# Optimization experiments

Hardware: AMD Instinct MI355X
Metric: run time of the kernel (lower is better)

Reference implementation:

```python
import jax, jax.numpy as jnp
import numpy as np
import math

H_HEADS = 16
D_PER = 64
D_MODEL = 1024
B, L = 8, 1024


def _dual_attention(q1, k1, q2, k2, v):
    # all [B,h,L,d]; scores = avg of two scaled QK^T
    scale = 1.0 / math.sqrt(q1.shape[-1])
    s1 = jnp.einsum('bhqd,bhkd->bhqk', q1, k1) * scale
    s2 = jnp.einsum('bhqd,bhkd->bhqk', q2, k2) * scale
    p = jax.nn.softmax((s1 + s2) * 0.5, axis=-1)
    return jnp.einsum('bhqk,bhkd->bhqd', p, v)


def _proj(X, W, b):
    # [B,L,D] -> [B,h,L,d]
    Bb, Ll, _ = X.shape
    y = X @ W + b
    return y.reshape(Bb, Ll, H_HEADS, D_PER).transpose(0, 2, 1, 3)


def _mha(Q1, K1, Q2, K2, V, Wq, bq, Wk, bk, Wv, bv, Wo, bo):
    q1 = _proj(Q1, Wq, bq)
    k1 = _proj(K1, Wk, bk)
    q2 = _proj(Q2, Wq, bq)  # same linear as q1 (linears[0])
    k2 = _proj(K2, Wk, bk)  # same linear as k1 (linears[1])
    v = _proj(V, Wv, bv)
    o = _dual_attention(q1, k1, q2, k2, v)  # [B,h,L,d]
    Bb = o.shape[0]
    o = o.transpose(0, 2, 1, 3).reshape(Bb, -1, H_HEADS * D_PER)
    return o @ Wo + bo  # [B,L,D]


def setup_inputs() -> dict:
    key = jax.random.key(0)
    ks = jax.random.split(key, 5)
    sc = 1.0 / math.sqrt(D_MODEL)
    return {
        'x': jax.random.normal(ks[0], (B, L, 3, D_MODEL), jnp.float32),
        'Wq': jax.random.normal(ks[1], (D_MODEL, H_HEADS * D_PER), jnp.float32) * sc,
        'bq': jnp.zeros((H_HEADS * D_PER,), jnp.float32),
        'Wk': jax.random.normal(ks[2], (D_MODEL, H_HEADS * D_PER), jnp.float32) * sc,
        'bk': jnp.zeros((H_HEADS * D_PER,), jnp.float32),
        'Wv': jax.random.normal(ks[3], (D_MODEL, H_HEADS * D_PER), jnp.float32) * sc,
        'bv': jnp.zeros((H_HEADS * D_PER,), jnp.float32),
        'Wo': jax.random.normal(ks[4], (H_HEADS * D_PER, D_MODEL), jnp.float32) * sc,
        'bo': jnp.zeros((D_MODEL,), jnp.float32),
    }


def reference(x, Wq, bq, Wk, bk, Wv, bv, Wo, bo):
    Hx = x[:, :, 0, :]
    Tx = x[:, :, 1, :]
    Rx = x[:, :, 2, :]
    p = (Wq, bq, Wk, bk, Wv, bv, Wo, bo)
    H_new = _mha(Tx, Tx, Rx, Rx, Hx, *p)
    T_new = _mha(Hx, Hx, Rx, Rx, Tx, *p)
    R_new = _mha(Hx, Hx, Tx, Tx, Rx, *p)
    return jnp.stack([H_new, T_new, R_new], axis=2)  # [B,L,3,D]
```

## Files before the change

kernel.cpp:

```cpp
#include <hip/hip_runtime.h>
#include <hip/hip_bf16.h>
#include <stdint.h>

#define NTOK 8192
#define DM   1024

typedef __bf16 bf16x8 __attribute__((ext_vector_type(8)));
typedef float  f32x4  __attribute__((ext_vector_type(4)));

__device__ __forceinline__ unsigned short f2bf(float f) {
  union { float f; unsigned u; } v; v.f = f;
  unsigned r = v.u + 0x7FFFu + ((v.u >> 16) & 1u);
  return (unsigned short)(r >> 16);
}

__device__ __forceinline__ void gld16(const void* g, const void* l) {
  __builtin_amdgcn_global_load_lds(
      (const __attribute__((address_space(1))) uint32_t*)g,
      (__attribute__((address_space(3))) uint32_t*)l, 16, 0, 0);
}

__global__ void convert_x(const float* __restrict__ x, unsigned short* __restrict__ Xbf) {
  int idx = (blockIdx.x * 256 + threadIdx.x) * 4;
  int s   = idx >> 23;
  int rem = idx & ((1 << 23) - 1);
  int tok = rem >> 10;
  int d   = rem & 1023;
  const float4 v = *(const float4*)&x[((size_t)tok * 3 + s) * 1024 + d];
  ushort4 o;
  o.x = f2bf(v.x); o.y = f2bf(v.y); o.z = f2bf(v.z); o.w = f2bf(v.w);
  *(ushort4*)&Xbf[idx] = o;
}

__global__ void transpose_w(const float* __restrict__ W, unsigned short* __restrict__ Wt) {
  __shared__ float t[32][33];
  int tx = threadIdx.x, ty = threadIdx.y;
  int bx = blockIdx.x * 32, by = blockIdx.y * 32;
#pragma unroll
  for (int i = 0; i < 32; i += 8)
    t[ty + i][tx] = W[(size_t)(by + ty + i) * 1024 + bx + tx];
  __syncthreads();
#pragma unroll
  for (int i = 0; i < 32; i += 8)
    Wt[(size_t)(bx + ty + i) * 1024 + by + tx] = f2bf(t[tx][ty + i]);
}

__device__ __forceinline__ void gemm128_core(
    const unsigned short* __restrict__ A, const unsigned short* __restrict__ Bt,
    unsigned short* lA, unsigned short* lB, f32x4 acc[4][4])
{
  int tid  = threadIdx.x;
  int wave = tid >> 6, lane = tid & 63, quad = lane >> 4, l16 = lane & 15;
  int m0 = blockIdx.x * 128, n0 = blockIdx.y * 128;
  int r0 = tid >> 2;
  int kc = (((tid & 3) ^ ((tid >> 3) & 3)) * 8);
  const unsigned short* Ag = A  + (size_t)(m0 + r0) * 1024 + kc;
  const unsigned short* Bg = Bt + (size_t)(n0 + r0) * 1024 + kc;
  int wm = (wave >> 1) * 64, wn = (wave & 1) * 64;
  int fsw = (l16 >> 1) & 3;

  for (int k0 = 0; k0 < 1024; k0 += 32) {
    gld16(Ag + k0,             lA + wave * 512);
    gld16(Ag + k0 + 64 * 1024, lA + 2048 + wave * 512);
    gld16(Bg + k0,             lB + wave * 512);
    gld16(Bg + k0 + 64 * 1024, lB + 2048 + wave * 512);
    __syncthreads();
    bf16x8 af[4], bfr[4];
    int fo = ((quad ^ fsw) * 8);
#pragma unroll
    for (int i = 0; i < 4; i++) {
      af[i]  = *(const bf16x8*)&lA[(wm + i * 16 + l16) * 32 + fo];
      bfr[i] = *(const bf16x8*)&lB[(wn + i * 16 + l16) * 32 + fo];
    }
#pragma unroll
    for (int mi = 0; mi < 4; mi++)
#pragma unroll
      for (int ni = 0; ni < 4; ni++)
        acc[mi][ni] = __builtin_amdgcn_mfma_f32_16x16x32_bf16(af[mi], bfr[ni], acc[mi][ni], 0, 0, 0);
    __syncthreads();
  }
}

__global__ __launch_bounds__(256, 2) void gemm_proj(
    const unsigned short* __restrict__ Xbf, const unsigned short* __restrict__ Wt,
    unsigned short* __restrict__ P,
    const float* __restrict__ bq, const float* __restrict__ bk, const float* __restrict__ bv)
{
  __shared__ alignas(16) unsigned short lA[128 * 32];
  __shared__ alignas(16) unsigned short lB[128 * 32];
  int z = blockIdx.z, s = z / 3, w = z - s * 3;
  const float* bias = (w == 0) ? bq : (w == 1) ? bk : bv;
  f32x4 acc[4][4];
#pragma unroll
  for (int i = 0; i < 4; i++)
#pragma unroll
    for (int j = 0; j < 4; j++) acc[i][j] = (f32x4){0.f, 0.f, 0.f, 0.f};
  gemm128_core(Xbf + (size_t)s * NTOK * 1024, Wt + (size_t)w * 1024 * 1024, lA, lB, acc);

  int tid = threadIdx.x, wave = tid >> 6, lane = tid & 63, quad = lane >> 4, l16 = lane & 15;
  int m0 = blockIdx.x * 128 + (wave >> 1) * 64;
  int n0 = blockIdx.y * 128 + (wave & 1) * 64;
  unsigned short* C = P + (size_t)z * NTOK * 1024;
  if (w == 2) {
#pragma unroll
    for (int mi = 0; mi < 4; mi++) {
      int row0 = m0 + mi * 16 + quad * 4;
      int b = row0 >> 10, l0 = row0 & 1023;
#pragma unroll
      for (int ni = 0; ni < 4; ni++) {
        int col = n0 + ni * 16 + l16;
        float bcol = bias[col];
        int hh = col >> 6, d = col & 63;
        ushort4 o4;
        o4.x = f2bf(acc[mi][ni][0] + bcol);
        o4.y = f2bf(acc[mi][ni][1] + bcol);
        o4.z = f2bf(acc[mi][ni][2] + bcol);
        o4.w = f2bf(acc[mi][ni][3] + bcol);
        *(ushort4*)&C[(size_t)(b * 16 + hh) * 65536 + (size_t)d * 1024 + l0] = o4;
      }
    }
  } else {
#pragma unroll
    for (int mi = 0; mi < 4; mi++)
#pragma unroll
      for (int ni = 0; ni < 4; ni++) {
        int col = n0 + ni * 16 + l16;
        float bcol = bias[col];
#pragma unroll
        for (int r = 0; r < 4; r++) {
          int row = m0 + mi * 16 + quad * 4 + r;
          C[(size_t)row * 1024 + col] = f2bf(acc[mi][ni][r] + bcol);
        }
      }
  }
}

__global__ __launch_bounds__(256, 4) void attn(
    const unsigned short* __restrict__ P, unsigned short* __restrict__ Oa)
{
  __shared__ alignas(16) unsigned short lK1[64 * 64];
  __shared__ alignas(16) unsigned short lK2[64 * 64];
  __shared__ alignas(16) unsigned short lV [64 * 64];
  __shared__ alignas(16) unsigned short pls[4][32 * 40];
  int o  = blockIdx.z;
  int As = (o == 0) ? 1 : 0;
  int Bs = (o == 2) ? 1 : 2;
  int b = blockIdx.x >> 4, h = blockIdx.x & 15;
  int tid = threadIdx.x, wave = tid >> 6, lane = tid & 63, quad = lane >> 4, l16 = lane & 15;
  int q0 = blockIdx.y * 128 + wave * 32;
  size_t bh_off = (size_t)b * 1024 * 1024 + h * 64;
  const unsigned short* Q1 = P + (size_t)(As * 3 + 0) * NTOK * 1024 + bh_off;
  const unsigned short* K1 = P + (size_t)(As * 3 + 1) * NTOK * 1024 + bh_off;
  const unsigned short* Q2 = P + (size_t)(Bs * 3 + 0) * NTOK * 1024 + bh_off;
  const unsigned short* K2 = P + (size_t)(Bs * 3 + 1) * NTOK * 1024 + bh_off;
  const unsigned short* V  = P + (size_t)(o * 3 + 2) * NTOK * 1024
                               + (size_t)(b * 16 + h) * 65536;
  unsigned short* myp = pls[wave];

  bf16x8 q1f[2][2], q2f[2][2];
#pragma unroll
  for (int qt = 0; qt < 2; qt++)
#pragma unroll
    for (int c = 0; c < 2; c++) {
      q1f[qt][c] = *(const bf16x8*)&Q1[(size_t)(q0 + qt * 16 + l16) * 1024 + c * 32 + quad * 8];
      q2f[qt][c] = *(const bf16x8*)&Q2[(size_t)(q0 + qt * 16 + l16) * 1024 + c * 32 + quad * 8];
    }
  bf16x8 ones;
#pragma unroll
  for (int j = 0; j < 8; j++) ones[j] = (__bf16)1.0f;

  int r8 = lane >> 3;
  int cs = ((lane & 7) ^ r8) * 8;
  int srow = wave * 16 + r8;
  const unsigned short* K1s = K1 + (size_t)srow * 1024 + cs;
  const unsigned short* K2s = K2 + (size_t)srow * 1024 + cs;
  const unsigned short* Vs  = V  + (size_t)srow * 1024 + cs;
  int fsw = (l16 & 7);

  f32x4 oacc[2][4];
#pragma unroll
  for (int qt = 0; qt < 2; qt++)
#pragma unroll
    for (int dt = 0; dt < 4; dt++) oacc[qt][dt] = (f32x4){0.f, 0.f, 0.f, 0.f};
  f32x4 lsum[2];
  lsum[0] = (f32x4){0.f, 0.f, 0.f, 0.f};
  lsum[1] = (f32x4){0.f, 0.f, 0.f, 0.f};

  const float SC = 0.09016844136867f;

  for (int k0 = 0; k0 < 1024; k0 += 64) {
#pragma unroll
    for (int half = 0; half < 2; half++) {
      size_t krow = (size_t)(k0 + half * 8) * 1024;
      gld16(K1s + krow,                 lK1 + (wave * 16 + half * 8) * 64);
      gld16(K2s + krow,                 lK2 + (wave * 16 + half * 8) * 64);
      gld16(Vs + k0 + half * 8 * 1024,  lV  + (wave * 16 + half * 8) * 64);
    }
    __syncthreads();

#pragma unroll
    for (int kc = 0; kc < 2; kc++) {
      f32x4 sacc[2][2];
      sacc[0][0] = (f32x4){0.f, 0.f, 0.f, 0.f};
      sacc[0][1] = (f32x4){0.f, 0.f, 0.f, 0.f};
      sacc[1][0] = (f32x4){0.f, 0.f, 0.f, 0.f};
      sacc[1][1] = (f32x4){0.f, 0.f, 0.f, 0.f};
      __builtin_amdgcn_s_setprio(1);
#pragma unroll
      for (int kt = 0; kt < 2; kt++) {
        int krow = (kc * 32 + kt * 16 + l16) * 64;
        bf16x8 k1a = *(const bf16x8*)&lK1[krow + ((quad ^ fsw) * 8)];
        bf16x8 k1b = *(const bf16x8*)&lK1[krow + (((quad + 4) ^ fsw) * 8)];
        bf16x8 k2a = *(const bf16x8*)&lK2[krow + ((quad ^ fsw) * 8)];
        bf16x8 k2b = *(const bf16x8*)&lK2[krow + (((quad + 4) ^ fsw) * 8)];
#pragma unroll
        for (int qt = 0; qt < 2; qt++) {
          sacc[qt][kt] = __builtin_amdgcn_mfma_f32_16x16x32_bf16(q1f[qt][0], k1a, sacc[qt][kt], 0, 0, 0);
          sacc[qt][kt] = __builtin_amdgcn_mfma_f32_16x16x32_bf16(q1f[qt][1], k1b, sacc[qt][kt], 0, 0, 0);
          sacc[qt][kt] = __builtin_amdgcn_mfma_f32_16x16x32_bf16(q2f[qt][0], k2a, sacc[qt][kt], 0, 0, 0);
          sacc[qt][kt] = __builtin_amdgcn_mfma_f32_16x16x32_bf16(q2f[qt][1], k2b, sacc[qt][kt], 0, 0, 0);
        }
      }
      __builtin_amdgcn_s_setprio(0);
#pragma unroll
      for (int qt = 0; qt < 2; qt++)
#pragma unroll
        for (int kt = 0; kt < 2; kt++)
#pragma unroll
          for (int r2 = 0; r2 < 2; r2++) {
            union { float f; unsigned u; } e0, e1;
            e0.f = __builtin_amdgcn_exp2f(sacc[qt][kt][r2 * 2]     * SC);
            e1.f = __builtin_amdgcn_exp2f(sacc[qt][kt][r2 * 2 + 1] * SC);
            unsigned pk = __builtin_amdgcn_perm(e1.u + 0x8000u, e0.u + 0x8000u, 0x07060302u);
            int row = qt * 16 + quad * 4 + r2 * 2;
            myp[row * 40 + kt * 16 + l16]       = (unsigned short)pk;
            myp[(row + 1) * 40 + kt * 16 + l16] = (unsigned short)(pk >> 16);
          }
      bf16x8 pa0 = *(const bf16x8*)&myp[l16 * 40 + quad * 8];
      bf16x8 pa1 = *(const bf16x8*)&myp[(16 + l16) * 40 + quad * 8];
      __builtin_amdgcn_s_setprio(1);
      lsum[0] = __builtin_amdgcn_mfma_f32_16x16x32_bf16(pa0, ones, lsum[0], 0, 0, 0);
      lsum[1] = __builtin_amdgcn_mfma_f32_16x16x32_bf16(pa1, ones, lsum[1], 0, 0, 0);
#pragma unroll
      for (int dt = 0; dt < 4; dt++) {
        bf16x8 vf = *(const bf16x8*)&lV[(dt * 16 + l16) * 64 + (((kc * 4 + quad) ^ fsw) * 8)];
        oacc[0][dt] = __builtin_amdgcn_mfma_f32_16x16x32_bf16(pa0, vf, oacc[0][dt], 0, 0, 0);
        oacc[1][dt] = __builtin_amdgcn_mfma_f32_16x16x32_bf16(pa1, vf, oacc[1][dt], 0, 0, 0);
      }
      __builtin_amdgcn_s_setprio(0);
    }
    __syncthreads();
  }

  unsigned short* Od = Oa + (size_t)o * NTOK * 1024 + bh_off;
#pragma unroll
  for (int qt = 0; qt < 2; qt++) {
    f32x4 inv;
#pragma unroll
    for (int r = 0; r < 4; r++) inv[r] = 1.0f / lsum[qt][r];
#pragma unroll
    for (int dt = 0; dt < 4; dt++)
#pragma unroll
      for (int r = 0; r < 4; r++) {
        float val = oacc[qt][dt][r] * inv[r];
        Od[(size_t)(q0 + qt * 16 + quad * 4 + r) * 1024 + dt * 16 + l16] = f2bf(val);
      }
  }
}

__global__ __launch_bounds__(256, 2) void gemm_out(
    const unsigned short* __restrict__ Oattn, const unsigned short* __restrict__ WtO,
    float* __restrict__ out, const float* __restrict__ bo)
{
  __shared__ alignas(16) unsigned short lA[128 * 32];
  __shared__ alignas(16) unsigned short lB[128 * 32];
  int s = blockIdx.z;
  f32x4 acc[4][4];
#pragma unroll
  for (int i = 0; i < 4; i++)
#pragma unroll
    for (int j = 0; j < 4; j++) acc[i][j] = (f32x4){0.f, 0.f, 0.f, 0.f};
  gemm128_core(Oattn + (size_t)s * NTOK * 1024, WtO, lA, lB, acc);

  int tid = threadIdx.x, wave = tid >> 6, lane = tid & 63, quad = lane >> 4, l16 = lane & 15;
  int m0 = blockIdx.x * 128 + (wave >> 1) * 64;
  int n0 = blockIdx.y * 128 + (wave & 1) * 64;
#pragma unroll
  for (int mi = 0; mi < 4; mi++)
#pragma unroll
    for (int ni = 0; ni < 4; ni++) {
      int col = n0 + ni * 16 + l16;
      float bcol = bo[col];
#pragma unroll
      for (int r = 0; r < 4; r++) {
        int row = m0 + mi * 16 + quad * 4 + r;
        out[(size_t)row * 3072 + s * 1024 + col] = acc[mi][ni][r] + bcol;
      }
    }
}

extern "C" void kernel_launch(void* const* d_in, const int* in_sizes, int n_in,
                              void* d_out, int out_size, void* d_ws, size_t ws_size,
                              hipStream_t stream) {
  (void)in_sizes; (void)n_in; (void)out_size; (void)ws_size;
  const float* x  = (const float*)d_in[0];
  const float* Wq = (const float*)d_in[1];
  const float* bq = (const float*)d_in[2];
  const float* Wk = (const float*)d_in[3];
  const float* bk = (const float*)d_in[4];
  const float* Wv = (const float*)d_in[5];
  const float* bv = (const float*)d_in[6];
  const float* Wo = (const float*)d_in[7];
  const float* bo = (const float*)d_in[8];
  float* out = (float*)d_out;

  char* ws = (char*)d_ws;
  unsigned short* Xbf = (unsigned short*)(ws + 0);
  unsigned short* Wt  = (unsigned short*)(ws + 50331648);
  unsigned short* P   = (unsigned short*)(ws + 58720256);
  unsigned short* Oa  = (unsigned short*)(ws + 209715200);

  convert_x<<<24576, 256, 0, stream>>>(x, Xbf);
  dim3 tb(32, 8), tg(32, 32);
  transpose_w<<<tg, tb, 0, stream>>>(Wq, Wt + 0 * 1048576);
  transpose_w<<<tg, tb, 0, stream>>>(Wk, Wt + 1 * 1048576);
  transpose_w<<<tg, tb, 0, stream>>>(Wv, Wt + 2 * 1048576);
  transpose_w<<<tg, tb, 0, stream>>>(Wo, Wt + 3 * 1048576);

  gemm_proj<<<dim3(64, 8, 9), 256, 0, stream>>>(Xbf, Wt, P, bq, bk, bv);
  attn<<<dim3(128, 8, 3), 256, 0, stream>>>(P, Oa);
  gemm_out<<<dim3(64, 8, 3), 256, 0, stream>>>(Oa, Wt + 3 * 1048576, out, bo);
}
```

Before: 614.2 us.

## Replace 128x128 GEMM core with pipelined 256x256 eight-wave tile core

Both projection and output GEMMs now use a 256x256 tile with 512 threads, K-step 64, double-buffered LDS staging via global_load_lds, and an interleaved schedule of LDS reads, async prefetches and MFMA quarters separated by barriers with raised wave priority. Blocks are also remapped with a swizzle to improve L2 reuse of A/B panels. The aim is to raise arithmetic intensity per LDS/global load and hide load latency behind MFMA work, at the cost of 128KB LDS per block, heavy register pressure, and fragile hand-tuned waitcnt/barrier ordering.

```diff
diff --git a/kernel.cpp b/kernel.cpp
--- a/kernel.cpp
+++ b/kernel.cpp
@@ -45,70 +45,130 @@
     Wt[(size_t)(bx + ty + i) * 1024 + by + tx] = f2bf(t[tx][ty + i]);
 }
 
-__device__ __forceinline__ void gemm128_core(
+#define STG_A(tt, d, hf) do { \
+  gld16(Ag + (size_t)((hf) * 128) * 1024 + (tt) * 64,      &lds[((d)*2+(hf))*8192 + wave*512]); \
+  gld16(Ag + (size_t)((hf) * 128 + 64) * 1024 + (tt) * 64, &lds[((d)*2+(hf))*8192 + wave*512 + 4096]); \
+} while (0)
+#define STG_B(tt, d, hf) do { \
+  gld16(Bg + (size_t)((hf) * 128) * 1024 + (tt) * 64,      &lds[32768 + ((d)*2+(hf))*8192 + wave*512]); \
+  gld16(Bg + (size_t)((hf) * 128 + 64) * 1024 + (tt) * 64, &lds[32768 + ((d)*2+(hf))*8192 + wave*512 + 4096]); \
+} while (0)
+#define RD_AG(g, d) do { \
+  const unsigned short* _p = &lds[((d)*2 + wm) * 8192]; \
+  _Pragma("unroll") for (int m2 = 0; m2 < 4; ++m2) \
+  _Pragma("unroll") for (int ks = 0; ks < 2; ++ks) \
+    af[(g)*4 + m2][ks] = *(const bf16x8*)&_p[((g)*4 + m2)*1024 + l16*64 + (((ks*4 + quad) ^ sw8) * 8)]; \
+} while (0)
+#define RD_BG(g, d) do { \
+  const unsigned short* _p = &lds[32768 + ((d)*2 + (wn >> 1)) * 8192 + (wn & 1) * 4096]; \
+  _Pragma("unroll") for (int n2 = 0; n2 < 2; ++n2) \
+  _Pragma("unroll") for (int ks = 0; ks < 2; ++ks) \
+    bfr[(g)*2 + n2][ks] = *(const bf16x8*)&_p[((g)*2 + n2)*1024 + l16*64 + (((ks*4 + quad) ^ sw8) * 8)]; \
+} while (0)
+#define MM_Q(qm, qn) do { \
+  __builtin_amdgcn_s_setprio(1); \
+  _Pragma("unroll") for (int m2 = 0; m2 < 4; ++m2) \
+  _Pragma("unroll") for (int n2 = 0; n2 < 2; ++n2) \
+  _Pragma("unroll") for (int ks = 0; ks < 2; ++ks) \
+    acc[(qm)*4 + m2][(qn)*2 + n2] = __builtin_amdgcn_mfma_f32_16x16x32_bf16( \
+      af[(qm)*4 + m2][ks], bfr[(qn)*2 + n2][ks], acc[(qm)*4 + m2][(qn)*2 + n2], 0, 0, 0); \
+  __builtin_amdgcn_s_setprio(0); \
+} while (0)
+#define PBAR() do { __builtin_amdgcn_s_barrier(); __builtin_amdgcn_sched_barrier(0); } while (0)
+#define WLGK0() do { asm volatile("s_waitcnt lgkmcnt(0)" ::: "memory"); __builtin_amdgcn_sched_barrier(0); } while (0)
+
+__device__ __forceinline__ void gemm256_core(
     const unsigned short* __restrict__ A, const unsigned short* __restrict__ Bt,
-    unsigned short* lA, unsigned short* lB, f32x4 acc[4][4])
+    unsigned short* lds, f32x4 acc[8][4], int m0, int n0)
 {
-  int tid  = threadIdx.x;
+  int tid = threadIdx.x;
   int wave = tid >> 6, lane = tid & 63, quad = lane >> 4, l16 = lane & 15;
-  int m0 = blockIdx.x * 128, n0 = blockIdx.y * 128;
-  int r0 = tid >> 2;
-  int kc = (((tid & 3) ^ ((tid >> 3) & 3)) * 8);
-  const unsigned short* Ag = A  + (size_t)(m0 + r0) * 1024 + kc;
-  const unsigned short* Bg = Bt + (size_t)(n0 + r0) * 1024 + kc;
-  int wm = (wave >> 1) * 64, wn = (wave & 1) * 64;
-  int fsw = (l16 >> 1) & 3;
-
-  for (int k0 = 0; k0 < 1024; k0 += 32) {
-    gld16(Ag + k0,             lA + wave * 512);
-    gld16(Ag + k0 + 64 * 1024, lA + 2048 + wave * 512);
-    gld16(Bg + k0,             lB + wave * 512);
-    gld16(Bg + k0 + 64 * 1024, lB + 2048 + wave * 512);
-    __syncthreads();
-    bf16x8 af[4], bfr[4];
-    int fo = ((quad ^ fsw) * 8);
-#pragma unroll
-    for (int i = 0; i < 4; i++) {
-      af[i]  = *(const bf16x8*)&lA[(wm + i * 16 + l16) * 32 + fo];
-      bfr[i] = *(const bf16x8*)&lB[(wn + i * 16 + l16) * 32 + fo];
-    }
-#pragma unroll
-    for (int mi = 0; mi < 4; mi++)
-#pragma unroll
-      for (int ni = 0; ni < 4; ni++)
-        acc[mi][ni] = __builtin_amdgcn_mfma_f32_16x16x32_bf16(af[mi], bfr[ni], acc[mi][ni], 0, 0, 0);
-    __syncthreads();
+  int wm = wave >> 2, wn = wave & 3;
+  int sw8 = l16 & 7;
+  int srow = wave * 8 + (lane >> 3);
+  int schk = ((lane & 7) ^ (lane >> 3)) * 8;
+  const unsigned short* Ag = A  + (size_t)(m0 + srow) * 1024 + schk;
+  const unsigned short* Bg = Bt + (size_t)(n0 + srow) * 1024 + schk;
+  bf16x8 af[8][2], bfr[4][2];
+
+  STG_A(0, 0, 0); STG_A(0, 0, 1); STG_B(0, 0, 0); STG_B(0, 0, 1);
+  STG_A(1, 1, 0); STG_A(1, 1, 1); STG_B(1, 1, 0);
+  asm volatile("s_waitcnt vmcnt(6)" ::: "memory");
+  PBAR();
+
+  for (int t = 0; t < 16; t += 2) {
+    RD_AG(0, 0); RD_BG(0, 0);
+    STG_B(t + 1, 1, 1);
+    __builtin_amdgcn_s_barrier(); WLGK0();
+    MM_Q(0, 0);
+    PBAR();
+    RD_AG(1, 0);
+    __builtin_amdgcn_s_barrier(); WLGK0();
+    MM_Q(1, 0);
+    PBAR();
+    RD_BG(1, 0);
+    if (t + 2 < 16) { STG_A(t + 2, 0, 0); STG_A(t + 2, 0, 1); }
+    __builtin_amdgcn_s_barrier(); WLGK0();
+    MM_Q(0, 1);
+    PBAR();
+    if (t + 2 < 16) STG_B(t + 2, 0, 0);
+    __builtin_amdgcn_s_barrier(); __builtin_amdgcn_sched_barrier(0);
+    MM_Q(1, 1);
+    if (t + 2 < 16) { asm volatile("s_waitcnt vmcnt(6)" ::: "memory"); }
+    else            { asm volatile("s_waitcnt vmcnt(0)" ::: "memory"); }
+    PBAR();
+    RD_AG(0, 1); RD_BG(0, 1);
+    if (t + 2 < 16) STG_B(t + 2, 0, 1);
+    __builtin_amdgcn_s_barrier(); WLGK0();
+    MM_Q(0, 0);
+    PBAR();
+    RD_AG(1, 1);
+    __builtin_amdgcn_s_barrier(); WLGK0();
+    MM_Q(1, 0);
+    PBAR();
+    RD_BG(1, 1);
+    if (t + 3 < 16) { STG_A(t + 3, 1, 0); STG_A(t + 3, 1, 1); }
+    __builtin_amdgcn_s_barrier(); WLGK0();
+    MM_Q(0, 1);
+    PBAR();
+    if (t + 3 < 16) STG_B(t + 3, 1, 0);
+    __builtin_amdgcn_s_barrier(); __builtin_amdgcn_sched_barrier(0);
+    MM_Q(1, 1);
+    if (t + 3 < 16) { asm volatile("s_waitcnt vmcnt(6)" ::: "memory"); }
+    PBAR();
   }
 }
 
-__global__ __launch_bounds__(256, 2) void gemm_proj(
+__global__ __launch_bounds__(512, 2) void gemm_proj(
     const unsigned short* __restrict__ Xbf, const unsigned short* __restrict__ Wt,
     unsigned short* __restrict__ P,
     const float* __restrict__ bq, const float* __restrict__ bk, const float* __restrict__ bv)
 {
-  __shared__ alignas(16) unsigned short lA[128 * 32];
-  __shared__ alignas(16) unsigned short lB[128 * 32];
+  __shared__ alignas(16) unsigned short lds[65536];
   int z = blockIdx.z, s = z / 3, w = z - s * 3;
   const float* bias = (w == 0) ? bq : (w == 1) ? bk : bv;
-  f32x4 acc[4][4];
-#pragma unroll
-  for (int i = 0; i < 4; i++)
+  int f = blockIdx.x;
+  int swz = (f & 7) * 16 + (f >> 3);
+  int m0 = (swz & 31) * 256, n0 = (swz >> 5) * 256;
+  f32x4 acc[8][4];
+#pragma unroll
+  for (int i = 0; i < 8; i++)
 #pragma unroll
     for (int j = 0; j < 4; j++) acc[i][j] = (f32x4){0.f, 0.f, 0.f, 0.f};
-  gemm128_core(Xbf + (size_t)s * NTOK * 1024, Wt + (size_t)w * 1024 * 1024, lA, lB, acc);
+  gemm256_core(Xbf + (size_t)s * NTOK * 1024, Wt + (size_t)w * 1048576, lds, acc, m0, n0);
 
   int tid = threadIdx.x, wave = tid >> 6, lane = tid & 63, quad = lane >> 4, l16 = lane & 15;
-  int m0 = blockIdx.x * 128 + (wave >> 1) * 64;
-  int n0 = blockIdx.y * 128 + (wave & 1) * 64;
+  int wm = wave >> 2, wn = wave & 3;
+  int rbase = m0 + wm * 128, cbase = n0 + wn * 64;
   unsigned short* C = P + (size_t)z * NTOK * 1024;
   if (w == 2) {
 #pragma unroll
-    for (int mi = 0; mi < 4; mi++) {
-      int row0 = m0 + mi * 16 + quad * 4;
+    for (int mi = 0; mi < 8; mi++) {
+      int row0 = rbase + mi * 16 + quad * 4;
       int b = row0 >> 10, l0 = row0 & 1023;
 #pragma unroll
       for (int ni = 0; ni < 4; ni++) {
-        int col = n0 + ni * 16 + l16;
+        int col = cbase + ni * 16 + l16;
         float bcol = bias[col];
         int hh = col >> 6, d = col & 63;
         ushort4 o4;
@@ -121,18 +181,51 @@
     }
   } else {
 #pragma unroll
-    for (int mi = 0; mi < 4; mi++)
+    for (int mi = 0; mi < 8; mi++)
 #pragma unroll
       for (int ni = 0; ni < 4; ni++) {
-        int col = n0 + ni * 16 + l16;
+        int col = cbase + ni * 16 + l16;
         float bcol = bias[col];
 #pragma unroll
         for (int r = 0; r < 4; r++) {
-          int row = m0 + mi * 16 + quad * 4 + r;
+          int row = rbase + mi * 16 + quad * 4 + r;
           C[(size_t)row * 1024 + col] = f2bf(acc[mi][ni][r] + bcol);
         }
       }
   }
+}
+
+__global__ __launch_bounds__(512, 2) void gemm_out(
+    const unsigned short* __restrict__ Oattn, const unsigned short* __restrict__ WtO,
+    float* __restrict__ out, const float* __restrict__ bo)
+{
+  __shared__ alignas(16) unsigned short lds[65536];
+  int s = blockIdx.z;
+  int f = blockIdx.x;
+  int swz = (f & 7) * 16 + (f >> 3);
+  int m0 = (swz & 31) * 256, n0 = (swz >> 5) * 256;
+  f32x4 acc[8][4];
+#pragma unroll
+  for (int i = 0; i < 8; i++)
+#pragma unroll
+    for (int j = 0; j < 4; j++) acc[i][j] = (f32x4){0.f, 0.f, 0.f, 0.f};
+  gemm256_core(Oattn + (size_t)s * NTOK * 1024, WtO, lds, acc, m0, n0);
+
+  int tid = threadIdx.x, wave = tid >> 6, lane = tid & 63, quad = lane >> 4, l16 = lane & 15;
+  int wm = wave >> 2, wn = wave & 3;
+  int rbase = m0 + wm * 128, cbase = n0 + wn * 64;
+#pragma unroll
+  for (int mi = 0; mi < 8; mi++)
+#pragma unroll
+    for (int ni = 0; ni < 4; ni++) {
+      int col = cbase + ni * 16 + l16;
+      float bcol = bo[col];
+#pragma unroll
+      for (int r = 0; r < 4; r++) {
+        int row = rbase + mi * 16 + quad * 4 + r;
+        out[(size_t)row * 3072 + s * 1024 + col] = acc[mi][ni][r] + bcol;
+      }
+    }
 }
 
 __global__ __launch_bounds__(256, 4) void attn(
@@ -268,37 +361,6 @@
   }
 }
 
-__global__ __launch_bounds__(256, 2) void gemm_out(
-    const unsigned short* __restrict__ Oattn, const unsigned short* __restrict__ WtO,
-    float* __restrict__ out, const float* __restrict__ bo)
-{
-  __shared__ alignas(16) unsigned short lA[128 * 32];
-  __shared__ alignas(16) unsigned short lB[128 * 32];
-  int s = blockIdx.z;
-  f32x4 acc[4][4];
-#pragma unroll
-  for (int i = 0; i < 4; i++)
-#pragma unroll
-    for (int j = 0; j < 4; j++) acc[i][j] = (f32x4){0.f, 0.f, 0.f, 0.f};
-  gemm128_core(Oattn + (size_t)s * NTOK * 1024, WtO, lA, lB, acc);
-
-  int tid = threadIdx.x, wave = tid >> 6, lane = tid & 63, quad = lane >> 4, l16 = lane & 15;
-  int m0 = blockIdx.x * 128 + (wave >> 1) * 64;
-  int n0 = blockIdx.y * 128 + (wave & 1) * 64;
-#pragma unroll
-  for (int mi = 0; mi < 4; mi++)
-#pragma unroll
-    for (int ni = 0; ni < 4; ni++) {
-      int col = n0 + ni * 16 + l16;
-      float bcol = bo[col];
-#pragma unroll
-      for (int r = 0; r < 4; r++) {
-        int row = m0 + mi * 16 + quad * 4 + r;
-        out[(size_t)row * 3072 + s * 1024 + col] = acc[mi][ni][r] + bcol;
-      }
-    }
-}
-
 extern "C" void kernel_launch(void* const* d_in, const int* in_sizes, int n_in,
                               void* d_out, int out_size, void* d_ws, size_t ws_size,
                               hipStream_t stream) {
@@ -327,7 +389,7 @@
   transpose_w<<<tg, tb, 0, stream>>>(Wv, Wt + 2 * 1048576);
   transpose_w<<<tg, tb, 0, stream>>>(Wo, Wt + 3 * 1048576);
 
-  gemm_proj<<<dim3(64, 8, 9), 256, 0, stream>>>(Xbf, Wt, P, bq, bk, bv);
+  gemm_proj<<<dim3(128, 1, 9), 512, 0, stream>>>(Xbf, Wt, P, bq, bk, bv);
   attn<<<dim3(128, 8, 3), 256, 0, stream>>>(P, Oa);
-  gemm_out<<<dim3(64, 8, 3), 256, 0, stream>>>(Oa, Wt + 3 * 1048576, out, bo);
-}
+  gemm_out<<<dim3(128, 1, 3), 512, 0, stream>>>(Oa, Wt + 3 * 1048576, out, bo);
+}
```

Result: no change. 613.5 us (-0.1%).
